# Performance work log

Measured on AMD Instinct MI355X. Metric: run time of the kernel, lower is better.

The kernel has to match this reference:

```python
import jax, jax.numpy as jnp
import numpy as np

N = 50000
E = 800000
IN_CH = 128
HID = 32
HEADS = 4
OUT_CH = 2
NEG_SLOPE = 0.2


def setup_inputs() -> dict:
    key = jax.random.key(0)
    ks = jax.random.split(key, 10)
    x = jax.random.normal(ks[0], (N, IN_CH), dtype=jnp.float32)
    edge_index = jax.random.randint(ks[1], (2, E), 0, N, dtype=jnp.int32)
    s1 = 1.0 / np.sqrt(IN_CH)
    s2 = 1.0 / np.sqrt(HEADS * HID)
    return {
        "x": x,
        "edge_index": edge_index,
        "W1": jax.random.normal(ks[2], (IN_CH, HEADS * HID), dtype=jnp.float32) * s1,
        "a_src1": jax.random.normal(ks[3], (HEADS, HID), dtype=jnp.float32) * s2,
        "a_dst1": jax.random.normal(ks[4], (HEADS, HID), dtype=jnp.float32) * s2,
        "b1": jnp.zeros((HEADS * HID,), dtype=jnp.float32),
        "W2": jax.random.normal(ks[5], (HEADS * HID, 1 * OUT_CH), dtype=jnp.float32) * s2,
        "a_src2": jax.random.normal(ks[6], (1, OUT_CH), dtype=jnp.float32),
        "a_dst2": jax.random.normal(ks[7], (1, OUT_CH), dtype=jnp.float32),
        "b2": jnp.zeros((OUT_CH,), dtype=jnp.float32),
    }


def gat_layer(x, edge_index, W, a_src, a_dst, bias, heads, out_ch, concat):
    # PyG GATConv: linear -> per-node attn terms -> per-edge LeakyReLU ->
    # softmax over incoming edges (self-loops added) -> scatter-add aggregate.
    n = x.shape[0]
    loop = jnp.arange(n, dtype=edge_index.dtype)
    src = jnp.concatenate([edge_index[0], loop])  # [E+N]
    dst = jnp.concatenate([edge_index[1], loop])
    h = (x @ W).reshape(n, heads, out_ch)                 # [N, H, C]
    a_s = jnp.einsum('nhc,hc->nh', h, a_src)              # [N, H]
    a_d = jnp.einsum('nhc,hc->nh', h, a_dst)
    e = jax.nn.leaky_relu(a_s[src] + a_d[dst], NEG_SLOPE)  # [E+N, H]
    m = jax.ops.segment_max(e, dst, num_segments=n)
    m = jax.lax.stop_gradient(jnp.where(jnp.isfinite(m), m, 0.0))
    p = jnp.exp(e - m[dst])
    denom = jax.ops.segment_sum(p, dst, num_segments=n)
    alpha = p / (denom[dst] + 1e-16)                       # softmax per dst node
    msg = h[src] * alpha[:, :, None]                       # [E+N, H, C]
    out = jax.ops.segment_sum(msg, dst, num_segments=n)    # [N, H, C]
    out = out.reshape(n, heads * out_ch) if concat else out.mean(axis=1)
    return out + bias


def reference(x, edge_index, W1, a_src1, a_dst1, b1, W2, a_src2, a_dst2, b2):
    h = gat_layer(x, edge_index, W1, a_src1, a_dst1, b1, HEADS, HID, True)
    h = jax.nn.relu(h)  # dropout is identity in eval mode
    o = gat_layer(h, edge_index, W2, a_src2, a_dst2, b2, 1, OUT_CH, False)
    return jax.nn.log_softmax(o, axis=1)
```

## Files before the change

kernel.cpp:

```cpp
#include <hip/hip_runtime.h>
#include <hip/hip_bf16.h>

#define NEG_SLOPE 0.2f
#define INV_LN2 1.44269504088896340736f
#define BSH   6
#define BUKSZ 64
#define MAXBUK 1024
#define CHUNK 4096
#define XPAD  136

typedef __attribute__((ext_vector_type(8))) short bf16x8;
typedef __attribute__((ext_vector_type(4))) float f32x4;

__device__ __forceinline__ float exp2lrelu(float z) {
    return __builtin_amdgcn_exp2f(fmaxf(z, NEG_SLOPE * z));
}

__device__ __forceinline__ unsigned short f2bf(float f) {
    unsigned int u = __float_as_uint(f);
    u = (u + 0x7fffu + ((u >> 16) & 1u)) >> 16;
    return (unsigned short)u;
}

__device__ __forceinline__ float2 bfpair(unsigned int u) {
    float2 r;
    r.x = __uint_as_float(u << 16);
    r.y = __uint_as_float(u & 0xffff0000u);
    return r;
}

__global__ __launch_bounds__(256) void k1_fat(const float* __restrict__ x,
                                              const float* __restrict__ W1,
                                              const float* __restrict__ a_src1,
                                              const float* __restrict__ a_dst1,
                                              unsigned short* __restrict__ h1b,
                                              float* __restrict__ a_s1,
                                              float* __restrict__ a_d1, int n,
                                              const int* __restrict__ e_dst, int e,
                                              int nbuk, int nblk,
                                              int* __restrict__ mat) {
    __shared__ unsigned short xsh[64 * XPAD];
    __shared__ unsigned short wsh[128 * XPAD];
    const int tid = threadIdx.x;

    if (blockIdx.x < (unsigned)nblk) {
        int* lcnt = (int*)xsh;
        const int bid = blockIdx.x;
        for (int b = tid; b < nbuk; b += 256) lcnt[b] = 0;
        __syncthreads();
        const int e0 = bid * CHUNK;
        const int e1 = min(e, e0 + CHUNK);
        for (int k = e0 + tid; k < e1; k += 256)
            atomicAdd(&lcnt[e_dst[k] >> BSH], 1);
        __syncthreads();
        for (int b = tid; b < nbuk; b += 256)
            mat[bid * nbuk + b] = lcnt[b];
        return;
    }

    const int row0 = (blockIdx.x - nblk) * 64;
    for (int i = tid; i < 128 * 128; i += 256) {
        int k = i >> 7, nn = i & 127;
        wsh[nn * XPAD + k] = f2bf(W1[i]);
    }
#pragma unroll
    for (int i = 0; i < 8; ++i) {
        int idx = tid + i * 256;
        int r = idx >> 5;
        int c = (idx & 31) * 4;
        int gr = row0 + r;
        float4 v = make_float4(0.f, 0.f, 0.f, 0.f);
        if (gr < n) v = *(const float4*)&x[(size_t)gr * 128 + c];
        ushort4 b;
        b.x = f2bf(v.x); b.y = f2bf(v.y); b.z = f2bf(v.z); b.w = f2bf(v.w);
        *(ushort4*)&xsh[r * XPAD + c] = b;
    }
    __syncthreads();

    const int wave = tid >> 6;
    const int lane = tid & 63;
    const int quad = lane >> 4;
    const int l16 = lane & 15;

    bf16x8 afrag[4];
#pragma unroll
    for (int ks = 0; ks < 4; ++ks)
        afrag[ks] = *(const bf16x8*)&xsh[(wave * 16 + l16) * XPAD + ks * 32 + quad * 8];

    f32x4 acc[8];
#pragma unroll
    for (int t = 0; t < 8; ++t) acc[t] = (f32x4){0.f, 0.f, 0.f, 0.f};

#pragma unroll
    for (int t = 0; t < 8; ++t) {
#pragma unroll
        for (int ks = 0; ks < 4; ++ks) {
            bf16x8 bfrag = *(const bf16x8*)&wsh[(t * 16 + l16) * XPAD + ks * 32 + quad * 8];
            acc[t] = __builtin_amdgcn_mfma_f32_16x16x32_bf16(afrag[ks], bfrag, acc[t], 0, 0, 0);
        }
    }

    float hs[4][4], hd[4][4];
#pragma unroll
    for (int h = 0; h < 4; ++h)
#pragma unroll
        for (int r = 0; r < 4; ++r) { hs[h][r] = 0.f; hd[h][r] = 0.f; }
#pragma unroll
    for (int t = 0; t < 8; ++t) {
        float as = a_src1[t * 16 + l16];
        float advv = a_dst1[t * 16 + l16];
#pragma unroll
        for (int r = 0; r < 4; ++r) {
            hs[t >> 1][r] += acc[t][r] * as;
            hd[t >> 1][r] += acc[t][r] * advv;
        }
    }
#pragma unroll
    for (int h = 0; h < 4; ++h)
#pragma unroll
        for (int r = 0; r < 4; ++r) {
            float ps = hs[h][r];
            float pd = hd[h][r];
#pragma unroll
            for (int off = 1; off < 16; off <<= 1) {
                ps += __shfl_xor(ps, off);
                pd += __shfl_xor(pd, off);
            }
            hs[h][r] = ps;
            hd[h][r] = pd;
        }
    if (l16 < 4) {
        int h = l16;
#pragma unroll
        for (int r = 0; r < 4; ++r) {
            int gr = row0 + wave * 16 + quad * 4 + r;
            if (gr < n) {
                a_s1[gr * 4 + h] = hs[h][r] * INV_LN2;
                a_d1[gr * 4 + h] = hd[h][r] * INV_LN2;
            }
        }
    }

    __syncthreads();
#pragma unroll
    for (int t = 0; t < 8; ++t)
#pragma unroll
        for (int r = 0; r < 4; ++r)
            xsh[(wave * 16 + quad * 4 + r) * XPAD + t * 16 + l16] = f2bf(acc[t][r]);
    __syncthreads();
#pragma unroll
    for (int i = 0; i < 8; ++i) {
        int idx = tid + i * 256;
        int r = idx >> 5;
        int c = (idx & 31) * 4;
        int gr = row0 + r;
        if (gr < n)
            *(ushort4*)&h1b[(size_t)gr * 128 + c] = *(ushort4*)&xsh[r * XPAD + c];
    }
}

__global__ __launch_bounds__(256) void kc_colscan(int* __restrict__ mat, int nbuk, int nblk,
                                                  int* __restrict__ btot) {
    int b = blockIdx.x * 256 + threadIdx.x;
    if (b >= nbuk) return;
    int run = 0;
#pragma unroll 4
    for (int i = 0; i < nblk; ++i) {
        int idx = i * nbuk + b;
        int t = mat[idx];
        mat[idx] = run;
        run += t;
    }
    btot[b] = run;
}

__global__ __launch_bounds__(256) void kb_place2(const int* __restrict__ src,
                                                 const int* __restrict__ dst, int e,
                                                 int nbuk, const int* __restrict__ mat,
                                                 const int* __restrict__ btot,
                                                 unsigned int* __restrict__ part,
                                                 int* __restrict__ bbase) {
    __shared__ int lbase[MAXBUK];
    __shared__ int s[256];
    const int tid = threadIdx.x;
    const int bid = blockIdx.x;
    int t4 = tid * 4;
    int v0 = (t4     < nbuk) ? btot[t4]     : 0;
    int v1 = (t4 + 1 < nbuk) ? btot[t4 + 1] : 0;
    int v2 = (t4 + 2 < nbuk) ? btot[t4 + 2] : 0;
    int v3 = (t4 + 3 < nbuk) ? btot[t4 + 3] : 0;
    int ssum = v0 + v1 + v2 + v3;
    s[tid] = ssum;
    __syncthreads();
    for (int off = 1; off < 256; off <<= 1) {
        int t = (tid >= off) ? s[tid - off] : 0;
        __syncthreads();
        s[tid] += t;
        __syncthreads();
    }
    int excl = s[tid] - ssum;
    if (t4 < nbuk)     lbase[t4]     = excl;
    if (t4 + 1 < nbuk) lbase[t4 + 1] = excl + v0;
    if (t4 + 2 < nbuk) lbase[t4 + 2] = excl + v0 + v1;
    if (t4 + 3 < nbuk) lbase[t4 + 3] = excl + v0 + v1 + v2;
    __syncthreads();
    if (bid == 0) {
        for (int b = tid; b < nbuk; b += 256) bbase[b] = lbase[b];
        if (tid == 255) bbase[nbuk] = s[255];
    }
    for (int b = tid; b < nbuk; b += 256)
        lbase[b] += mat[bid * nbuk + b];
    __syncthreads();
    const int e0 = bid * CHUNK;
    const int e1 = min(e, e0 + CHUNK);
    for (int k = e0 + tid; k < e1; k += 256) {
        int d = dst[k];
        int pos = atomicAdd(&lbase[d >> BSH], 1);
        part[pos] = ((unsigned int)src[k] << 16) | (unsigned int)(d & 0xffff);
    }
}

__global__ __launch_bounds__(256) void kc_csr(const unsigned int* __restrict__ part,
                                              const int* __restrict__ bbase, int nbuk,
                                              int* __restrict__ row_start,
                                              unsigned short* __restrict__ csr_src) {
    __shared__ int cnt[64];
    __shared__ int cur[64];
    const int b = blockIdx.x;
    const int tid = threadIdx.x;
    const int eb = bbase[b];
    const int nE = bbase[b + 1] - eb;
    if (tid < 64) cnt[tid] = 0;
    __syncthreads();
    for (int k = tid; k < nE; k += 256)
        atomicAdd(&cnt[part[eb + k] & 63u], 1);
    __syncthreads();
    if (tid < 64) {
        int v = cnt[tid];
        int incl = v;
#pragma unroll
        for (int off = 1; off < 64; off <<= 1) {
            int t = __shfl_up(incl, off);
            if (tid >= off) incl += t;
        }
        int excl = incl - v;
        cur[tid] = excl;
        row_start[(b << BSH) + tid] = eb + excl;
        if (tid == 63 && b == nbuk - 1) row_start[(b << BSH) + 64] = eb + incl;
    }
    __syncthreads();
    for (int k = tid; k < nE; k += 256) {
        unsigned int u = part[eb + k];
        int pos = atomicAdd(&cur[u & 63u], 1);
        csr_src[eb + pos] = (unsigned short)(u >> 16);
    }
}

__global__ __launch_bounds__(256) void k3_agg1(
    const unsigned short* __restrict__ h1b, const float* __restrict__ a_s1,
    const float* __restrict__ a_d1, const int* __restrict__ row_start,
    const unsigned short* __restrict__ csr_src, const float* __restrict__ b1,
    const float* __restrict__ W2, const float* __restrict__ a_src2,
    const float* __restrict__ a_dst2, float4* __restrict__ pk, int n) {
    const int wid = (blockIdx.x * blockDim.x + threadIdx.x) >> 6;
    const int lane = threadIdx.x & 63;
    if (wid >= n) return;
    const int q = lane >> 4;
    const int l16 = lane & 15;
    const int c0 = l16 * 8;
    const unsigned cb = (unsigned)l16 * 16u;
    const int head = l16 >> 2;
    const int rs = row_start[wid];
    const int deg = row_start[wid + 1] - rs;
    const float ad = a_d1[wid * 4 + head];
    const char* __restrict__ h1c = (const char*)h1b;
    const unsigned short* __restrict__ crs = csr_src + rs;

    float dnm = 0.f;
    float acc[8] = {};
    const int dm1 = deg - 1;
    const int rounded = (deg + 15) & ~15;
    for (int j = q; j < rounded; j += 16) {
        int i0 = min(j,      dm1);
        int i1 = min(j + 4,  dm1);
        int i2 = min(j + 8,  dm1);
        int i3 = min(j + 12, dm1);
        unsigned s0 = (unsigned)crs[i0];
        unsigned s1 = (unsigned)crs[i1];
        unsigned s2 = (unsigned)crs[i2];
        unsigned s3 = (unsigned)crs[i3];
        float as0 = a_s1[(s0 << 2) + head];
        float as1 = a_s1[(s1 << 2) + head];
        float as2 = a_s1[(s2 << 2) + head];
        float as3 = a_s1[(s3 << 2) + head];
        uint4 g0 = *(const uint4*)(h1c + ((s0 << 8) + cb));
        uint4 g1 = *(const uint4*)(h1c + ((s1 << 8) + cb));
        uint4 g2 = *(const uint4*)(h1c + ((s2 << 8) + cb));
        uint4 g3 = *(const uint4*)(h1c + ((s3 << 8) + cb));
        float p0 = (j      < deg) ? exp2lrelu(as0 + ad) : 0.f;
        float p1 = (j + 4  < deg) ? exp2lrelu(as1 + ad) : 0.f;
        float p2 = (j + 8  < deg) ? exp2lrelu(as2 + ad) : 0.f;
        float p3 = (j + 12 < deg) ? exp2lrelu(as3 + ad) : 0.f;
        dnm += (p0 + p1) + (p2 + p3);
        float2 v0a = bfpair(g0.x), v0b = bfpair(g0.y), v0c = bfpair(g0.z), v0d = bfpair(g0.w);
        float2 v1a = bfpair(g1.x), v1b = bfpair(g1.y), v1c = bfpair(g1.z), v1d = bfpair(g1.w);
        float2 v2a = bfpair(g2.x), v2b = bfpair(g2.y), v2c = bfpair(g2.z), v2d = bfpair(g2.w);
        float2 v3a = bfpair(g3.x), v3b = bfpair(g3.y), v3c = bfpair(g3.z), v3d = bfpair(g3.w);
        acc[0] += (p0 * v0a.x + p1 * v1a.x) + (p2 * v2a.x + p3 * v3a.x);
        acc[1] += (p0 * v0a.y + p1 * v1a.y) + (p2 * v2a.y + p3 * v3a.y);
        acc[2] += (p0 * v0b.x + p1 * v1b.x) + (p2 * v2b.x + p3 * v3b.x);
        acc[3] += (p0 * v0b.y + p1 * v1b.y) + (p2 * v2b.y + p3 * v3b.y);
        acc[4] += (p0 * v0c.x + p1 * v1c.x) + (p2 * v2c.x + p3 * v3c.x);
        acc[5] += (p0 * v0c.y + p1 * v1c.y) + (p2 * v2c.y + p3 * v3c.y);
        acc[6] += (p0 * v0d.x + p1 * v1d.x) + (p2 * v2d.x + p3 * v3d.x);
        acc[7] += (p0 * v0d.y + p1 * v1d.y) + (p2 * v2d.y + p3 * v3d.y);
    }
    dnm += __shfl_xor(dnm, 16);
    dnm += __shfl_xor(dnm, 32);
#pragma unroll
    for (int k = 0; k < 8; ++k) {
        acc[k] += __shfl_xor(acc[k], 16);
        acc[k] += __shfl_xor(acc[k], 32);
    }
    {
        float p = exp2lrelu(a_s1[wid * 4 + head] + ad);
        uint4 g0 = *(const uint4*)(h1c + (((unsigned)wid << 8) + cb));
        float2 ha = bfpair(g0.x), hb = bfpair(g0.y), hc = bfpair(g0.z), hd2 = bfpair(g0.w);
        dnm += p;
        acc[0] += p * ha.x;  acc[1] += p * ha.y;
        acc[2] += p * hb.x;  acc[3] += p * hb.y;
        acc[4] += p * hc.x;  acc[5] += p * hc.y;
        acc[6] += p * hd2.x; acc[7] += p * hd2.y;
    }
    float inv = 1.f / (dnm + 1e-16f);
    float r[8];
    float4 bva = *(const float4*)&b1[c0];
    float4 bvb = *(const float4*)&b1[c0 + 4];
    r[0] = fmaxf(acc[0] * inv + bva.x, 0.f);
    r[1] = fmaxf(acc[1] * inv + bva.y, 0.f);
    r[2] = fmaxf(acc[2] * inv + bva.z, 0.f);
    r[3] = fmaxf(acc[3] * inv + bva.w, 0.f);
    r[4] = fmaxf(acc[4] * inv + bvb.x, 0.f);
    r[5] = fmaxf(acc[5] * inv + bvb.y, 0.f);
    r[6] = fmaxf(acc[6] * inv + bvb.z, 0.f);
    r[7] = fmaxf(acc[7] * inv + bvb.w, 0.f);

    float p0 = 0.f, p1 = 0.f;
#pragma unroll
    for (int k = 0; k < 4; ++k) {
        float4 w = *(const float4*)&W2[c0 * 2 + k * 4];
        p0 += r[2 * k] * w.x + r[2 * k + 1] * w.z;
        p1 += r[2 * k] * w.y + r[2 * k + 1] * w.w;
    }
#pragma unroll
    for (int off = 1; off < 16; off <<= 1) {
        p0 += __shfl_xor(p0, off);
        p1 += __shfl_xor(p1, off);
    }
    if (lane == 0) {
        pk[wid] = make_float4(p0, p1,
                              (p0 * a_src2[0] + p1 * a_src2[1]) * INV_LN2,
                              (p0 * a_dst2[0] + p1 * a_dst2[1]) * INV_LN2);
    }
}

__global__ __launch_bounds__(256) void k4_agg2(
    const float4* __restrict__ pk, const int* __restrict__ row_start,
    const unsigned short* __restrict__ csr_src, const float* __restrict__ b2,
    float* __restrict__ out, int n) {
    const int g = blockIdx.x * blockDim.x + threadIdx.x;
    const int lane = threadIdx.x & 63;
    const int node = (g >> 6) * 4 + (lane >> 4);
    const int l16 = lane & 15;
    if (node >= n) return;
    const int rs = row_start[node];
    const int deg = row_start[node + 1] - rs;
    const float4 me = pk[node];
    const float ad = me.w;

    float dnm = 0.f, a0 = 0.f, a1 = 0.f;
    for (int j = l16; j < deg; j += 16) {
        int s = (int)csr_src[rs + j];
        float4 qv = pk[s];
        float p = exp2lrelu(qv.z + ad);
        dnm += p;
        a0 += p * qv.x;
        a1 += p * qv.y;
    }
    if (l16 == 0) {
        float p = exp2lrelu(me.z + ad);
        dnm += p;
        a0 += p * me.x;
        a1 += p * me.y;
    }
#pragma unroll
    for (int off = 1; off < 16; off <<= 1) {
        dnm += __shfl_xor(dnm, off);
        a0 += __shfl_xor(a0, off);
        a1 += __shfl_xor(a1, off);
    }
    if (l16 == 0) {
        float inv = 1.f / (dnm + 1e-16f);
        float o0 = a0 * inv + b2[0];
        float o1 = a1 * inv + b2[1];
        float m2 = fmaxf(o0, o1);
        float lse = m2 + logf(__expf(o0 - m2) + __expf(o1 - m2));
        out[node * 2 + 0] = o0 - lse;
        out[node * 2 + 1] = o1 - lse;
    }
}

extern "C" void kernel_launch(void* const* d_in, const int* in_sizes, int n_in,
                              void* d_out, int out_size, void* d_ws, size_t ws_size,
                              hipStream_t stream) {
    const float* x      = (const float*)d_in[0];
    const int*   ei     = (const int*)d_in[1];
    const float* W1     = (const float*)d_in[2];
    const float* a_src1 = (const float*)d_in[3];
    const float* a_dst1 = (const float*)d_in[4];
    const float* b1     = (const float*)d_in[5];
    const float* W2     = (const float*)d_in[6];
    const float* a_src2 = (const float*)d_in[7];
    const float* a_dst2 = (const float*)d_in[8];
    const float* b2     = (const float*)d_in[9];
    float* out = (float*)d_out;

    const int N = in_sizes[0] / 128;
    const int E = in_sizes[1] / 2;
    const int* e_src = ei;
    const int* e_dst = ei + E;

    const int NBUK = (N + BUKSZ - 1) >> BSH;
    const int nblk = (E + CHUNK - 1) / CHUNK;
    const int gemmBlocks = (N + 63) / 64;

    char* p = (char*)d_ws;
    auto alloc = [&](size_t bytes) -> void* {
        void* r = (void*)p;
        p += (bytes + 255) & ~(size_t)255;
        return r;
    };
    unsigned short* h1b   = (unsigned short*)alloc((size_t)N * 128 * 2);
    float*          a_s1  = (float*)alloc((size_t)N * 4 * 4);
    float*          a_d1  = (float*)alloc((size_t)N * 4 * 4);
    float4*         pk    = (float4*)alloc((size_t)N * 16);
    int*            mat   = (int*)alloc((size_t)NBUK * nblk * 4);
    int*            btot  = (int*)alloc((size_t)NBUK * 4);
    int*            bbase = (int*)alloc((size_t)(NBUK + 1) * 4);
    unsigned int*   part  = (unsigned int*)alloc((size_t)E * 4);
    int*            row_start = (int*)alloc(((size_t)NBUK * BUKSZ + 1) * 4);
    unsigned short* csr_src   = (unsigned short*)alloc((size_t)E * 2);

    k1_fat<<<nblk + gemmBlocks, 256, 0, stream>>>(x, W1, a_src1, a_dst1, h1b, a_s1, a_d1, N,
                                                  e_dst, E, NBUK, nblk, mat);
    kc_colscan<<<(NBUK + 255) / 256, 256, 0, stream>>>(mat, NBUK, nblk, btot);
    kb_place2<<<nblk, 256, 0, stream>>>(e_src, e_dst, E, NBUK, mat, btot, part, bbase);
    kc_csr<<<NBUK, 256, 0, stream>>>(part, bbase, NBUK, row_start, csr_src);

    k3_agg1<<<(N * 64 + 255) / 256, 256, 0, stream>>>(h1b, a_s1, a_d1, row_start, csr_src,
                                                      b1, W2, a_src2, a_dst2, pk, N);
    k4_agg2<<<((N + 3) / 4 * 64 + 255) / 256, 256, 0, stream>>>(pk, row_start, csr_src,
                                                                b2, out, N);
}
```

Measured before the change: 202.7 us.

## Replace per-block count matrix and column scan with global atomic bucket counts

Per-chunk bucket counts are now accumulated into a global histogram with atomics, which removes the count matrix and the serial column-scan kernel. The placement kernel recounts its own chunk and claims a slot range per bucket via a global cursor atomic. A small prep kernel pre-converts and transposes W1 to bf16 once, so the GEMM blocks load it with vector copies instead of each converting it. CHUNK is halved to give more placement blocks. Edge order within a bucket is now nondeterministic, and the extra recount in placement adds reads of dst.

```diff
diff --git a/kernel.cpp b/kernel.cpp
--- a/kernel.cpp
+++ b/kernel.cpp
@@ -6,7 +6,7 @@
 #define BSH   6
 #define BUKSZ 64
 #define MAXBUK 1024
-#define CHUNK 4096
+#define CHUNK 2048
 #define XPAD  136
 
 typedef __attribute__((ext_vector_type(8))) short bf16x8;
@@ -29,8 +29,20 @@
     return r;
 }
 
+__global__ __launch_bounds__(256) void k0_prep(const float* __restrict__ W1,
+                                               unsigned short* __restrict__ w1t,
+                                               int* __restrict__ bcnt,
+                                               int* __restrict__ gcur, int nbuk) {
+    int g = blockIdx.x * 256 + threadIdx.x;
+    if (g < nbuk) { bcnt[g] = 0; gcur[g] = 0; }
+    if (g < 128 * 128) {
+        int k = g >> 7, nn = g & 127;
+        w1t[nn * 128 + k] = f2bf(W1[g]);
+    }
+}
+
 __global__ __launch_bounds__(256) void k1_fat(const float* __restrict__ x,
-                                              const float* __restrict__ W1,
+                                              const unsigned short* __restrict__ w1t,
                                               const float* __restrict__ a_src1,
                                               const float* __restrict__ a_dst1,
                                               unsigned short* __restrict__ h1b,
@@ -38,7 +50,7 @@
                                               float* __restrict__ a_d1, int n,
                                               const int* __restrict__ e_dst, int e,
                                               int nbuk, int nblk,
-                                              int* __restrict__ mat) {
+                                              int* __restrict__ bcnt) {
     __shared__ unsigned short xsh[64 * XPAD];
     __shared__ unsigned short wsh[128 * XPAD];
     const int tid = threadIdx.x;
@@ -53,15 +65,22 @@
         for (int k = e0 + tid; k < e1; k += 256)
             atomicAdd(&lcnt[e_dst[k] >> BSH], 1);
         __syncthreads();
-        for (int b = tid; b < nbuk; b += 256)
-            mat[bid * nbuk + b] = lcnt[b];
+        for (int b = tid; b < nbuk; b += 256) {
+            int c = lcnt[b];
+            if (c) atomicAdd(&bcnt[b], c);
+        }
         return;
     }
 
     const int row0 = (blockIdx.x - nblk) * 64;
-    for (int i = tid; i < 128 * 128; i += 256) {
-        int k = i >> 7, nn = i & 127;
-        wsh[nn * XPAD + k] = f2bf(W1[i]);
+    {
+        const bf16x8* w1v = (const bf16x8*)w1t;
+#pragma unroll
+        for (int ii = 0; ii < 8; ++ii) {
+            int i = tid + ii * 256;
+            int r = i >> 4, c = (i & 15) * 8;
+            *(bf16x8*)&wsh[r * XPAD + c] = w1v[i];
+        }
     }
 #pragma unroll
     for (int i = 0; i < 8; ++i) {
@@ -159,38 +178,25 @@
     }
 }
 
-__global__ __launch_bounds__(256) void kc_colscan(int* __restrict__ mat, int nbuk, int nblk,
-                                                  int* __restrict__ btot) {
-    int b = blockIdx.x * 256 + threadIdx.x;
-    if (b >= nbuk) return;
-    int run = 0;
-#pragma unroll 4
-    for (int i = 0; i < nblk; ++i) {
-        int idx = i * nbuk + b;
-        int t = mat[idx];
-        mat[idx] = run;
-        run += t;
-    }
-    btot[b] = run;
-}
-
-__global__ __launch_bounds__(256) void kb_place2(const int* __restrict__ src,
+__global__ __launch_bounds__(256) void kb_place3(const int* __restrict__ src,
                                                  const int* __restrict__ dst, int e,
-                                                 int nbuk, const int* __restrict__ mat,
-                                                 const int* __restrict__ btot,
+                                                 int nbuk, const int* __restrict__ bcnt,
+                                                 int* __restrict__ gcur,
                                                  unsigned int* __restrict__ part,
                                                  int* __restrict__ bbase) {
     __shared__ int lbase[MAXBUK];
+    __shared__ int lcur[MAXBUK];
     __shared__ int s[256];
     const int tid = threadIdx.x;
     const int bid = blockIdx.x;
     int t4 = tid * 4;
-    int v0 = (t4     < nbuk) ? btot[t4]     : 0;
-    int v1 = (t4 + 1 < nbuk) ? btot[t4 + 1] : 0;
-    int v2 = (t4 + 2 < nbuk) ? btot[t4 + 2] : 0;
-    int v3 = (t4 + 3 < nbuk) ? btot[t4 + 3] : 0;
+    int v0 = (t4     < nbuk) ? bcnt[t4]     : 0;
+    int v1 = (t4 + 1 < nbuk) ? bcnt[t4 + 1] : 0;
+    int v2 = (t4 + 2 < nbuk) ? bcnt[t4 + 2] : 0;
+    int v3 = (t4 + 3 < nbuk) ? bcnt[t4 + 3] : 0;
     int ssum = v0 + v1 + v2 + v3;
     s[tid] = ssum;
+    for (int b = tid; b < nbuk; b += 256) lcur[b] = 0;
     __syncthreads();
     for (int off = 1; off < 256; off <<= 1) {
         int t = (tid >= off) ? s[tid - off] : 0;
@@ -208,14 +214,19 @@
         for (int b = tid; b < nbuk; b += 256) bbase[b] = lbase[b];
         if (tid == 255) bbase[nbuk] = s[255];
     }
-    for (int b = tid; b < nbuk; b += 256)
-        lbase[b] += mat[bid * nbuk + b];
-    __syncthreads();
     const int e0 = bid * CHUNK;
     const int e1 = min(e, e0 + CHUNK);
+    for (int k = e0 + tid; k < e1; k += 256)
+        atomicAdd(&lcur[dst[k] >> BSH], 1);
+    __syncthreads();
+    for (int b = tid; b < nbuk; b += 256) {
+        int c = lcur[b];
+        if (c) lcur[b] = lbase[b] + atomicAdd(&gcur[b], c);
+    }
+    __syncthreads();
     for (int k = e0 + tid; k < e1; k += 256) {
         int d = dst[k];
-        int pos = atomicAdd(&lbase[d >> BSH], 1);
+        int pos = atomicAdd(&lcur[d >> BSH], 1);
         part[pos] = ((unsigned int)src[k] << 16) | (unsigned int)(d & 0xffff);
     }
 }
@@ -444,17 +455,18 @@
     float*          a_s1  = (float*)alloc((size_t)N * 4 * 4);
     float*          a_d1  = (float*)alloc((size_t)N * 4 * 4);
     float4*         pk    = (float4*)alloc((size_t)N * 16);
-    int*            mat   = (int*)alloc((size_t)NBUK * nblk * 4);
-    int*            btot  = (int*)alloc((size_t)NBUK * 4);
+    unsigned short* w1t   = (unsigned short*)alloc((size_t)128 * 128 * 2);
+    int*            bcnt  = (int*)alloc((size_t)NBUK * 4);
+    int*            gcur  = (int*)alloc((size_t)NBUK * 4);
     int*            bbase = (int*)alloc((size_t)(NBUK + 1) * 4);
     unsigned int*   part  = (unsigned int*)alloc((size_t)E * 4);
     int*            row_start = (int*)alloc(((size_t)NBUK * BUKSZ + 1) * 4);
     unsigned short* csr_src   = (unsigned short*)alloc((size_t)E * 2);
 
-    k1_fat<<<nblk + gemmBlocks, 256, 0, stream>>>(x, W1, a_src1, a_dst1, h1b, a_s1, a_d1, N,
-                                                  e_dst, E, NBUK, nblk, mat);
-    kc_colscan<<<(NBUK + 255) / 256, 256, 0, stream>>>(mat, NBUK, nblk, btot);
-    kb_place2<<<nblk, 256, 0, stream>>>(e_src, e_dst, E, NBUK, mat, btot, part, bbase);
+    k0_prep<<<64, 256, 0, stream>>>(W1, w1t, bcnt, gcur, NBUK);
+    k1_fat<<<nblk + gemmBlocks, 256, 0, stream>>>(x, w1t, a_src1, a_dst1, h1b, a_s1, a_d1, N,
+                                                  e_dst, E, NBUK, nblk, bcnt);
+    kb_place3<<<nblk, 256, 0, stream>>>(e_src, e_dst, E, NBUK, bcnt, gcur, part, bbase);
     kc_csr<<<NBUK, 256, 0, stream>>>(part, bbase, NBUK, row_start, csr_src);
 
     k3_agg1<<<(N * 64 + 255) / 256, 256, 0, stream>>>(h1b, a_s1, a_d1, row_start, csr_src,
```

Result: faster. 180.2 us (-11.1%).
